# Performance work log

Measured on AMD Instinct MI355X. Metric: run time of the kernel, lower is better.

The kernel has to match this reference:

```python
import jax, jax.numpy as jnp
import numpy as np

K = 20
NEG_SLOPE = 0.2
BN_EPS = 1e-5


def knn_idx(x, k):
    # x: (B, C, N) -> neighbor indices (B, N, k) by largest negative sq-distance
    xt = jnp.swapaxes(x, 1, 2)                      # (B, N, C)
    inner = 2.0 * jnp.einsum('bic,bjc->bij', xt, xt)
    sq = jnp.sum(xt * xt, axis=-1)                  # (B, N)
    dist = inner - sq[:, :, None] - sq[:, None, :]  # -||xi-xj||^2
    _, idx = jax.lax.top_k(dist, k)
    return idx


def edge_feature(x, src, idx):
    # x: (B, C, N) centers; src: (B, C, M) gather source; idx: (B, N, k)
    xt = jnp.swapaxes(x, 1, 2)                      # (B, N, C)
    st = jnp.swapaxes(src, 1, 2)                    # (B, M, C)
    b = jnp.arange(xt.shape[0])[:, None, None]
    neigh = st[b, idx]                              # (B, N, k, C)
    center = xt[:, :, None, :]                      # (B, N, 1, C)
    feat = jnp.concatenate(
        [neigh - center, jnp.broadcast_to(center, neigh.shape)], axis=-1)
    return jnp.transpose(feat, (0, 3, 1, 2))        # (B, 2C, N, k)


def conv_bn_lrelu(x, w, gamma, beta):
    # 1x1 conv (no bias) + training-mode BatchNorm2d + LeakyReLU(0.2)
    y = jnp.einsum('oc,bcnk->bonk', w, x)
    mean = jnp.mean(y, axis=(0, 2, 3), keepdims=True)
    var = jnp.var(y, axis=(0, 2, 3), keepdims=True)
    y = (y - mean) * jax.lax.rsqrt(var + BN_EPS)
    y = y * gamma[None, :, None, None] + beta[None, :, None, None]
    return jnp.where(y >= 0, y, NEG_SLOPE * y)


def knn_ia_idx(x, y, k):
    # cosine-similarity KNN from x (B,Cx,N) into y (B,Cy,M), normalize over channels
    xn = x / jnp.maximum(jnp.linalg.norm(x, axis=1, keepdims=True), 1e-12)
    yn = y / jnp.maximum(jnp.linalg.norm(y, axis=1, keepdims=True), 1e-12)
    simi = jnp.einsum('bci,bcj->bij', xn, yn)       # (B, N, M)
    _, idx = jax.lax.top_k(simi, k)
    return idx


def setup_inputs() -> dict:
    key = jax.random.key(0)
    ks = jax.random.split(key, 8)
    B, N, M, EMB = 8, 1024, 1024, 512
    x = jax.random.normal(ks[0], (B, 3, N), dtype=jnp.float32)
    y = jax.random.normal(ks[1], (B, 128, M), dtype=jnp.float32)
    def w(k_, o, c):
        return jax.random.normal(k_, (o, c), dtype=jnp.float32) * (1.0 / np.sqrt(c))
    inp = {
        'x': x, 'y': y,
        'w1': w(ks[2], 64, 6),
        'w2': w(ks[3], 64, 128),
        'w3': w(ks[4], 128, 128),
        'w4': w(ks[5], 256, 256),
        'w5': w(ks[6], EMB, 512),
        'g1': jnp.ones(64), 'b1': jnp.zeros(64),
        'g2': jnp.ones(64), 'b2': jnp.zeros(64),
        'g3': jnp.ones(128), 'b3': jnp.zeros(128),
        'g4': jnp.ones(256), 'b4': jnp.zeros(256),
        'g5': jnp.ones(EMB), 'b5': jnp.zeros(EMB),
    }
    return inp


def reference(x, y, w1, w2, w3, w4, w5, g1, b1, g2, b2, g3, b3, g4, b4, g5, b5):
    # block 1
    h = conv_bn_lrelu(edge_feature(x, x, knn_idx(x, K)), w1, g1, b1)
    x1 = jnp.max(h, axis=-1)                        # (B, 64, N)
    # block 2
    h = conv_bn_lrelu(edge_feature(x1, x1, knn_idx(x1, K)), w2, g2, b2)
    x2 = jnp.max(h, axis=-1)                        # (B, 64, N)
    # block 3
    h = conv_bn_lrelu(edge_feature(x2, x2, knn_idx(x2, K)), w3, g3, b3)
    x3 = jnp.max(h, axis=-1)                        # (B, 128, N)
    # block 4: cross-attention KNN into y (cosine similarity)
    h = conv_bn_lrelu(edge_feature(x3, y, knn_ia_idx(x3, y, K)), w4, g4, b4)
    x4 = jnp.max(h, axis=-1)                        # (B, 256, N)
    # final 1x1 conv + BN + LeakyReLU on concatenated features (512 ch)
    cat = jnp.concatenate([x1, x2, x3, x4], axis=1)  # (B, 512, N)
    out = conv_bn_lrelu(cat[..., None], w5, g5, b5)[..., 0]
    return out                                       # (B, n_emb_dims, N)
```

## Files before the change

kernel.cpp:

```cpp
#include <hip/hip_runtime.h>
#include <hip/hip_bf16.h>

#define KNN 20
#define NEG_SLOPE 0.2f

constexpr int BB = 8;
constexpr int NN = 1024;
constexpr int MM = 1024;

typedef short bf16x8 __attribute__((ext_vector_type(8)));
typedef float f32x4 __attribute__((ext_vector_type(4)));
typedef double f64x4 __attribute__((ext_vector_type(4)));
typedef unsigned long long u64;

__device__ __forceinline__ u64 pack_key64(double d, int j) {
  u64 u = (u64)__double_as_longlong(d);
  u = (u & 0x8000000000000000ULL) ? ~u : (u | 0x8000000000000000ULL);
  return (u & ~(u64)1023) | (u64)(1023 - j);
}

__device__ __forceinline__ void topk20_u64(u64 (&s)[16], int lane, int* op) {
#pragma unroll
  for (int p = 1; p < 16; p <<= 1) {
#pragma unroll
    for (int k = p; k >= 1; k >>= 1) {
#pragma unroll
      for (int j = k % p; j + k < 16; j += 2 * k) {
#pragma unroll
        for (int i = 0; i < k; ++i) {
          int a = j + i, b = j + i + k;
          if (b < 16 && (a / (2 * p)) == (b / (2 * p))) {
            u64 hi = s[a] > s[b] ? s[a] : s[b];
            u64 lo = s[a] > s[b] ? s[b] : s[a];
            s[a] = hi;
            s[b] = lo;
          }
        }
      }
    }
  }
#pragma unroll
  for (int r = 0; r < KNN; ++r) {
    u64 win = s[0];
#pragma unroll
    for (int off = 32; off > 0; off >>= 1) {
      u64 o = __shfl_xor(win, off, 64);
      win = o > win ? o : win;
    }
    if (lane == 0) op[r] = 1023 - (int)(win & (u64)1023);
    if (s[0] == win) {
#pragma unroll
      for (int i = 0; i < 15; ++i) s[i] = s[i + 1];
      s[15] = 0ULL;
    }
  }
}

__global__ void k_probe_mfma(int* __restrict__ rowt, int* __restrict__ colt,
                             int* __restrict__ flag) {
  __shared__ int cnt[256];
  __shared__ int oksh;
  int tid = threadIdx.x;
  if (tid == 0) oksh = 1;
  for (int e = tid; e < 256; e += 64) cnt[e] = 0;
  __syncthreads();
  int lane = tid & 63;
  f64x4 z = {0.0, 0.0, 0.0, 0.0};
  double ai = (double)(lane & 15);
  double p3 = 1.0, p5 = 1.0;
  int kq = lane >> 4;
  for (int t = 0; t < kq; ++t) { p3 *= 3.0; p5 *= 5.0; }
  f64x4 d1 = __builtin_amdgcn_mfma_f64_16x16x4f64(ai, 1.0, z, 0, 0, 0);
  f64x4 d2 = __builtin_amdgcn_mfma_f64_16x16x4f64(1.0, ai, z, 0, 0, 0);
  f64x4 d3 = __builtin_amdgcn_mfma_f64_16x16x4f64(p3, p5, z, 0, 0, 0);
  bool ok = true;
  int ri[4], ci[4];
#pragma unroll
  for (int r = 0; r < 4; ++r) {
    double va = d1[r], vb = d2[r], vp = d3[r];
    int i = (int)(va * 0.25);
    int j = (int)(vb * 0.25);
    bool e_ok = (i >= 0) && (i < 16) && (j >= 0) && (j < 16) &&
                (va == 4.0 * (double)i) && (vb == 4.0 * (double)j) && (vp == 3616.0);
    if (e_ok) {
      atomicAdd(&cnt[i * 16 + j], 1);
    } else {
      ok = false;
      i = 0;
      j = 0;
    }
    ri[r] = i;
    ci[r] = j;
  }
  if (!ok) atomicExch(&oksh, 0);
  __syncthreads();
  bool bij = true;
  for (int e = tid; e < 256; e += 64)
    if (cnt[e] != 1) bij = false;
  if (!bij) atomicExch(&oksh, 0);
  __syncthreads();
#pragma unroll
  for (int r = 0; r < 4; ++r) {
    rowt[lane * 4 + r] = ri[r];
    colt[lane * 4 + r] = ci[r];
  }
  if (tid == 0) *flag = oksh;
}

__global__ __launch_bounds__(256) void k_transpose_d(
    const float* __restrict__ in, double* __restrict__ out, int C, int Np) {
  int total = BB * C * Np;
  for (int t = blockIdx.x * 256 + threadIdx.x; t < total; t += gridDim.x * 256) {
    int c = t % C;
    int n = (t / C) % Np;
    int b = t / (C * Np);
    out[t] = (double)in[((size_t)b * C + c) * Np + n];
  }
}

__global__ __launch_bounds__(256) void k_cvt_bf16(
    const float* __restrict__ in, __hip_bfloat16* __restrict__ out, int n) {
  int i = blockIdx.x * 256 + threadIdx.x;
  if (i < n) out[i] = __float2bfloat16(in[i]);
}

template <int RECIP>
__global__ __launch_bounds__(256) void k_rowsq(
    const double* __restrict__ A, int ld, int C, double* __restrict__ sq) {
  int p = blockIdx.x * 256 + threadIdx.x;
  if (p >= BB * NN) return;
  const double* row = A + (size_t)p * ld;
  double s = 0.0;
  for (int c = 0; c < C; ++c) { double v = row[c]; s += v * v; }
  if (RECIP) {
    sq[p] = 1.0 / fmax(sqrt(s), 1e-12);
  } else {
    sq[p] = s;
  }
}

__global__ __launch_bounds__(256) void k_knn3(
    const double* __restrict__ xs3, const double* __restrict__ sq, int* __restrict__ idx) {
  __shared__ double P[NN * 3];
  int b = blockIdx.x;
  const double* Xb = xs3 + (size_t)b * NN * 3;
  int tid = threadIdx.x;
  for (int t = tid; t < NN * 3; t += 256) P[t] = Xb[t];
  __syncthreads();
  int wave = tid >> 6, lane = tid & 63;
  int i = blockIdx.y * 4 + wave;
  double xi = P[i * 3], yi = P[i * 3 + 1], zi = P[i * 3 + 2];
  double sqi = sq[b * NN + i];
  u64 s[16];
#pragma unroll
  for (int m = 0; m < 16; ++m) {
    int j = m * 64 + lane;
    double d = fma(xi, P[j * 3], 0.0);
    d = fma(yi, P[j * 3 + 1], d);
    d = fma(zi, P[j * 3 + 2], d);
    s[m] = pack_key64(2.0 * d - sqi - sq[b * NN + j], j);
  }
  int* op = idx + ((size_t)b * NN + i) * KNN;
  topk20_u64(s, lane, op);
}

template <int MODE>
__global__ __launch_bounds__(64, 2) void k_gram_u(
    const double* __restrict__ A, int lda, const double* __restrict__ Bm, int ldb,
    const double* __restrict__ sqA, const double* __restrict__ sqB,
    u64* __restrict__ kk, int C, int b0, const int* __restrict__ rowt,
    const int* __restrict__ colt, const int* __restrict__ flag) {
  __shared__ double As[2][8][69];
  __shared__ double Bs[2][8][69];
  int bg = b0 + blockIdx.x;
  int bl = blockIdx.x;
  int j0 = blockIdx.y * 64;
  int i0 = blockIdx.z * 64;
  const double* Ab = A + (size_t)bg * NN * lda;
  const double* Bb = Bm + (size_t)bg * MM * ldb;
  int lane = threadIdx.x;
  if (*flag) {
    int lm = lane & 15, lq = lane >> 4;
    int k8 = lane & 7, r8 = lane >> 3;
    const double* pa = Ab + (size_t)(i0 + r8) * lda + k8;
    const double* pb = Bb + (size_t)(j0 + r8) * ldb + k8;
    f64x4 acc[4][4] = {};
    double ra[8], rb[8];
#pragma unroll
    for (int r = 0; r < 8; ++r) {
      ra[r] = pa[(size_t)(8 * r) * lda];
      rb[r] = pb[(size_t)(8 * r) * ldb];
    }
#pragma unroll
    for (int r = 0; r < 8; ++r) {
      As[0][k8][r8 + 8 * r] = ra[r];
      Bs[0][k8][r8 + 8 * r] = rb[r];
    }
    int nblk = C >> 3;
    for (int cb = 0; cb < nblk; ++cb) {
      int buf = cb & 1;
      bool pf = (cb + 1 < nblk);
      if (pf) {
        int c0 = (cb + 1) << 3;
#pragma unroll
        for (int r = 0; r < 8; ++r) {
          ra[r] = pa[(size_t)(8 * r) * lda + c0];
          rb[r] = pb[(size_t)(8 * r) * ldb + c0];
        }
      }
#pragma unroll
      for (int kc = 0; kc < 2; ++kc) {
        double a_[4], b_[4];
#pragma unroll
        for (int s = 0; s < 4; ++s) {
          a_[s] = As[buf][kc * 4 + lq][s * 16 + lm];
          b_[s] = Bs[buf][kc * 4 + lq][s * 16 + lm];
        }
#pragma unroll
        for (int si = 0; si < 4; ++si)
#pragma unroll
          for (int sj = 0; sj < 4; ++sj)
            acc[si][sj] = __builtin_amdgcn_mfma_f64_16x16x4f64(a_[si], b_[sj],
                                                               acc[si][sj], 0, 0, 0);
      }
      if (pf) {
        int nb = buf ^ 1;
#pragma unroll
        for (int r = 0; r < 8; ++r) {
          As[nb][k8][r8 + 8 * r] = ra[r];
          Bs[nb][k8][r8 + 8 * r] = rb[r];
        }
      }
    }
    int rta[4], cta[4];
#pragma unroll
    for (int r = 0; r < 4; ++r) {
      rta[r] = rowt[lane * 4 + r];
      cta[r] = colt[lane * 4 + r];
    }
#pragma unroll
    for (int si = 0; si < 4; ++si) {
#pragma unroll
      for (int sj = 0; sj < 4; ++sj) {
#pragma unroll
        for (int r = 0; r < 4; ++r) {
          int i = i0 + si * 16 + rta[r];
          int j = j0 + sj * 16 + cta[r];
          double v = acc[si][sj][r];
          if (MODE == 1)
            v = 2.0 * v - sqA[(size_t)bg * NN + i] - sqB[(size_t)bg * MM + j];
          if (MODE == 2) v = v * sqA[(size_t)bg * NN + i] * sqB[(size_t)bg * MM + j];
          kk[((size_t)bl * NN + i) * MM + j] = pack_key64(v, j);
        }
      }
    }
  } else {
    int lr = lane >> 3, lc = lane & 7;
    double acc2[8][8] = {};
    for (int c0 = 0; c0 < C; c0 += 8) {
      if (c0) __syncthreads();
      for (int r = 0; r < 8; ++r) {
        int li = lane + r * 64;
        int row = li >> 3, k = li & 7;
        As[0][k][row] = Ab[(size_t)(i0 + row) * lda + c0 + k];
        Bs[0][k][row] = Bb[(size_t)(j0 + row) * ldb + c0 + k];
      }
      __syncthreads();
#pragma unroll
      for (int k = 0; k < 8; ++k) {
        double a_[8], b_[8];
#pragma unroll
        for (int t = 0; t < 8; ++t) {
          a_[t] = As[0][k][lr * 8 + t];
          b_[t] = Bs[0][k][lc * 8 + t];
        }
#pragma unroll
        for (int ii = 0; ii < 8; ++ii)
#pragma unroll
          for (int jj = 0; jj < 8; ++jj)
            acc2[ii][jj] = fma(a_[ii], b_[jj], acc2[ii][jj]);
      }
    }
    for (int ii = 0; ii < 8; ++ii) {
      int i = i0 + lr * 8 + ii;
      double qa = sqA[(size_t)bg * NN + i];
      for (int jj = 0; jj < 8; ++jj) {
        int j = j0 + lc * 8 + jj;
        double v = acc2[ii][jj];
        if (MODE == 1) v = 2.0 * v - qa - sqB[(size_t)bg * MM + j];
        if (MODE == 2) v = v * qa * sqB[(size_t)bg * MM + j];
        kk[((size_t)bl * NN + i) * MM + j] = pack_key64(v, j);
      }
    }
  }
}

__global__ __launch_bounds__(256) void k_topk(const u64* __restrict__ kk,
                                              int* __restrict__ idx, int b0) {
  int wave = threadIdx.x >> 6;
  int lane = threadIdx.x & 63;
  int bl = blockIdx.x;
  int row = blockIdx.y * 4 + wave;
  const u64* rp = kk + ((size_t)bl * NN + row) * MM;
  u64 s[16];
#pragma unroll
  for (int m = 0; m < 16; ++m) s[m] = rp[m * 64 + lane];
  int* op = idx + ((size_t)(b0 + bl) * NN + row) * KNN;
  topk20_u64(s, lane, op);
}

__global__ __launch_bounds__(256) void k_featmm2(
    const double* __restrict__ src0, int ld0, int Np0,
    const double* __restrict__ src1, int ld1,
    const float* __restrict__ w, int CW,
    double* __restrict__ out0, double* __restrict__ out1, int C, int O,
    const int* __restrict__ rowt, const int* __restrict__ colt,
    const int* __restrict__ flag) {
  __shared__ double As[16][68];
  __shared__ double Ws[16][68];
  int nbo = O >> 6;
  int b = blockIdx.x;
  int mode = blockIdx.y >= nbo;
  int o0 = (blockIdx.y - (mode ? nbo : 0)) * 64;
  int j0 = blockIdx.z * 64;
  const double* src = mode ? src1 : src0;
  int lds_ = mode ? ld1 : ld0;
  int Np = mode ? NN : Np0;
  double* out = mode ? out1 : out0;
  int tid = threadIdx.x;
  const double* Sb = src + (size_t)b * Np * lds_;
  if (*flag) {
    int lane = tid & 63, wv = tid >> 6;
    int lm = lane & 15, lq = lane >> 4;
    f64x4 acc[4] = {};
    for (int c0 = 0; c0 < C; c0 += 16) {
      if (c0) __syncthreads();
      for (int r = 0; r < 4; ++r) {
        int li = tid + r * 256;
        int row = li >> 4, k = li & 15;
        int c = c0 + k;
        As[k][row] = (c < C) ? Sb[(size_t)(j0 + row) * lds_ + c] : 0.0;
        double wvv = 0.0;
        if (c < C) {
          const float* wr = w + (size_t)(o0 + row) * CW;
          wvv = (mode == 0) ? (double)wr[c] : ((double)wr[C + c] - (double)wr[c]);
        }
        Ws[k][row] = wvv;
      }
      __syncthreads();
#pragma unroll
      for (int kc = 0; kc < 4; ++kc) {
        double a = As[kc * 4 + lq][wv * 16 + lm];
#pragma unroll
        for (int t = 0; t < 4; ++t) {
          double bb = Ws[kc * 4 + lq][t * 16 + lm];
          acc[t] = __builtin_amdgcn_mfma_f64_16x16x4f64(a, bb, acc[t], 0, 0, 0);
        }
      }
    }
    int rta[4], cta[4];
#pragma unroll
    for (int r = 0; r < 4; ++r) {
      rta[r] = rowt[lane * 4 + r];
      cta[r] = colt[lane * 4 + r];
    }
#pragma unroll
    for (int t = 0; t < 4; ++t) {
#pragma unroll
      for (int r = 0; r < 4; ++r) {
        int j = j0 + wv * 16 + rta[r];
        int o = o0 + t * 16 + cta[r];
        out[((size_t)b * Np + j) * O + o] = acc[t][r];
      }
    }
  } else {
    int tx = tid & 15, ty = tid >> 4;
    double acc[4][4] = {};
    for (int c0 = 0; c0 < C; c0 += 16) {
      if (c0) __syncthreads();
      for (int r = 0; r < 4; ++r) {
        int li = tid + r * 256;
        int row = li >> 4, k = li & 15;
        int c = c0 + k;
        As[k][row] = (c < C) ? Sb[(size_t)(j0 + row) * lds_ + c] : 0.0;
        double wvv = 0.0;
        if (c < C) {
          const float* wr = w + (size_t)(o0 + row) * CW;
          wvv = (mode == 0) ? (double)wr[c] : ((double)wr[C + c] - (double)wr[c]);
        }
        Ws[k][row] = wvv;
      }
      __syncthreads();
#pragma unroll
      for (int k = 0; k < 16; ++k) {
        double a_[4], b_[4];
#pragma unroll
        for (int ii = 0; ii < 4; ++ii) a_[ii] = As[k][ty * 4 + ii];
#pragma unroll
        for (int jj = 0; jj < 4; ++jj) b_[jj] = Ws[k][tx * 4 + jj];
#pragma unroll
        for (int ii = 0; ii < 4; ++ii)
#pragma unroll
          for (int jj = 0; jj < 4; ++jj)
            acc[ii][jj] = fma(a_[ii], b_[jj], acc[ii][jj]);
      }
    }
    for (int ii = 0; ii < 4; ++ii) {
      int j = j0 + ty * 4 + ii;
      double* op = &out[((size_t)b * Np + j) * O + o0 + tx * 4];
      double2 v0, v1;
      v0.x = acc[ii][0];
      v0.y = acc[ii][1];
      v1.x = acc[ii][2];
      v1.y = acc[ii][3];
      *(double2*)op = v0;
      *(double2*)(op + 2) = v1;
    }
  }
}

__global__ __launch_bounds__(64, 2) void k_gemm5_mfma(
    const __hip_bfloat16* __restrict__ cath, const __hip_bfloat16* __restrict__ w5h,
    float* __restrict__ out) {
  int b = blockIdx.x;
  int j0 = blockIdx.y * 64;
  int o0 = blockIdx.z * 64;
  int lane = threadIdx.x;
  int m = lane & 15;
  int quad = lane >> 4;
  const __hip_bfloat16* arow = cath + ((size_t)(b * NN + j0 + m)) * 512 + quad * 8;
  const __hip_bfloat16* brow = w5h + ((size_t)(o0 + m)) * 512 + quad * 8;
  f32x4 acc[4][4] = {};
#pragma unroll
  for (int c0 = 0; c0 < 512; c0 += 32) {
    bf16x8 a[4], bb[4];
#pragma unroll
    for (int s = 0; s < 4; ++s) {
      a[s] = *(const bf16x8*)(arow + (size_t)s * 16 * 512 + c0);
      bb[s] = *(const bf16x8*)(brow + (size_t)s * 16 * 512 + c0);
    }
#pragma unroll
    for (int si = 0; si < 4; ++si)
#pragma unroll
      for (int sj = 0; sj < 4; ++sj)
        acc[si][sj] =
            __builtin_amdgcn_mfma_f32_16x16x32_bf16(a[si], bb[sj], acc[si][sj], 0, 0, 0);
  }
#pragma unroll
  for (int si = 0; si < 4; ++si) {
    float* ob = &out[((size_t)(b * NN + j0 + si * 16 + quad * 4)) * 512 + o0 + m];
#pragma unroll
    for (int sj = 0; sj < 4; ++sj)
#pragma unroll
      for (int r = 0; r < 4; ++r)
        ob[(size_t)r * 512 + sj * 16] = acc[si][sj][r];
  }
}

__global__ __launch_bounds__(256) void k_gather(
    const double* __restrict__ u, const double* __restrict__ t, const int* __restrict__ idx,
    double* __restrict__ stats, double* __restrict__ mx, int O, int srcNp) {
  __shared__ int lidx[16 * KNN];
  __shared__ double rs[256];
  __shared__ double rq[256];
  int b = blockIdx.x;
  int n0 = blockIdx.y * 16;
  int o0 = blockIdx.z * 64;
  int tid = threadIdx.x;
  int lane = tid & 63, nsl = tid >> 6;
  for (int w = tid; w < 16 * KNN; w += 256)
    lidx[w] = idx[((size_t)b * NN + n0) * KNN + w];
  __syncthreads();
  int oo = o0 + lane;
  double s1 = 0.0, s2 = 0.0;
  for (int ns = nsl; ns < 16; ns += 4) {
    size_t row = (size_t)b * NN + n0 + ns;
    double tv = t[row * O + oo];
    double mxv = -INFINITY;
    double a1 = 0.0, a2 = 0.0;
#pragma unroll
    for (int k = 0; k < KNN; ++k) {
      int j = lidx[ns * KNN + k];
      double yv = u[((size_t)b * srcNp + j) * O + oo] + tv;
      mxv = fmax(mxv, yv);
      a1 += yv;
      a2 = fma(yv, yv, a2);
    }
    mx[row * O + oo] = mxv;
    s1 += a1;
    s2 += a2;
  }
  rs[tid] = s1;
  rq[tid] = s2;
  __syncthreads();
  if (tid < 64) {
    s1 = rs[tid] + rs[tid + 64] + rs[tid + 128] + rs[tid + 192];
    s2 = rq[tid] + rq[tid + 64] + rq[tid + 128] + rq[tid + 192];
    atomicAdd(&stats[o0 + tid], s1);
    atomicAdd(&stats[O + o0 + tid], s2);
  }
}

__global__ __launch_bounds__(256) void k_bnapply(
    const double* __restrict__ mx, const double* __restrict__ u, const double* __restrict__ t,
    const int* __restrict__ idx, const double* __restrict__ stats,
    const float* __restrict__ gamma, const float* __restrict__ beta, double cnt,
    double* __restrict__ catd, __hip_bfloat16* __restrict__ cath, int coff, int O,
    int srcNp) {
  __shared__ double scs[256];
  __shared__ double scc[256];
  int tid = threadIdx.x;
  if (tid < O) {
    double mean = stats[tid] / cnt;
    double var = stats[O + tid] / cnt - mean * mean;
    if (var < 0.0) var = 0.0;
    double rstd = 1.0 / sqrt(var + 1e-5);
    double s = (double)gamma[tid] * rstd;
    scs[tid] = s;
    scc[tid] = (double)beta[tid] - mean * s;
  }
  __syncthreads();
  int i = blockIdx.x * 256 + tid;
  int total = BB * NN * O;
  if (i >= total) return;
  int oo = i % O;
  int n = (i / O) % NN;
  int b = i / (O * NN);
  double s = scs[oo], c = scc[oo];
  double v;
  if (s >= 0.0) {
    v = mx[i];
  } else {
    double tv = t[i];
    double mn = INFINITY;
    for (int k = 0; k < KNN; ++k) {
      int j = idx[((size_t)b * NN + n) * KNN + k];
      mn = fmin(mn, u[((size_t)b * srcNp + j) * O + oo] + tv);
    }
    v = mn;
  }
  double a = s * v + c;
  a = (a >= 0.0) ? a : 0.2 * a;
  size_t ci = ((size_t)b * NN + n) * 512 + coff + oo;
  cath[ci] = __float2bfloat16((float)a);
  if (coff < 256) catd[((size_t)b * NN + n) * 256 + coff + oo] = a;
}

__global__ __launch_bounds__(256) void k_stats512(
    const float* __restrict__ y5, double* __restrict__ stats) {
  int b = blockIdx.y;
  int n0 = blockIdx.x * 32;
  int tid = threadIdx.x;
  for (int part = 0; part < 2; ++part) {
    int oo = tid + part * 256;
    float a1 = 0.f, a2 = 0.f;
    for (int ns = 0; ns < 32; ++ns) {
      float v = y5[((size_t)b * NN + n0 + ns) * 512 + oo];
      a1 += v;
      a2 = fmaf(v, v, a2);
    }
    atomicAdd(&stats[oo], (double)a1);
    atomicAdd(&stats[512 + oo], (double)a2);
  }
}

__global__ __launch_bounds__(256) void k_final5b(
    const float* __restrict__ y5, const double* __restrict__ stats,
    const float* __restrict__ g5, const float* __restrict__ b5,
    float* __restrict__ out) {
  __shared__ float tile[64][65];
  __shared__ double scs[64];
  __shared__ double scc[64];
  int b = blockIdx.z;
  int n0 = blockIdx.x * 64;
  int o0 = blockIdx.y * 64;
  int tid = threadIdx.x;
  if (tid < 64) {
    int o = o0 + tid;
    double cnt = (double)(BB * NN);
    double mean = stats[o] / cnt;
    double var = stats[512 + o] / cnt - mean * mean;
    if (var < 0.0) var = 0.0;
    double rstd = 1.0 / sqrt(var + 1e-5);
    double s = (double)g5[o] * rstd;
    scs[tid] = s;
    scc[tid] = (double)b5[o] - mean * s;
  }
  __syncthreads();
  for (int r = 0; r < 16; ++r) {
    int li = tid + r * 256;
    int nl = li >> 6, ol = li & 63;
    float v = y5[((size_t)b * NN + n0 + nl) * 512 + o0 + ol];
    float a = (float)(scs[ol] * (double)v + scc[ol]);
    a = (a >= 0.f) ? a : NEG_SLOPE * a;
    tile[nl][ol] = a;
  }
  __syncthreads();
  for (int r = 0; r < 16; ++r) {
    int li = tid + r * 256;
    int ol = li >> 6, nl = li & 63;
    out[((size_t)b * 512 + o0 + ol) * NN + n0 + nl] = tile[nl][ol];
  }
}

extern "C" void kernel_launch(void* const* d_in, const int* in_sizes, int n_in,
                              void* d_out, int out_size, void* d_ws, size_t ws_size,
                              hipStream_t stream) {
  const float* x = (const float*)d_in[0];
  const float* y = (const float*)d_in[1];
  const float* w1 = (const float*)d_in[2];
  const float* w2 = (const float*)d_in[3];
  const float* w3 = (const float*)d_in[4];
  const float* w4 = (const float*)d_in[5];
  const float* w5 = (const float*)d_in[6];
  const float* g1 = (const float*)d_in[7];
  const float* b1 = (const float*)d_in[8];
  const float* g2 = (const float*)d_in[9];
  const float* b2 = (const float*)d_in[10];
  const float* g3 = (const float*)d_in[11];
  const float* b3 = (const float*)d_in[12];
  const float* g4 = (const float*)d_in[13];
  const float* b4 = (const float*)d_in[14];
  const float* g5 = (const float*)d_in[15];
  const float* b5 = (const float*)d_in[16];

  char* base = (char*)d_ws;
  size_t off = 0;
  auto alloc = [&](size_t bytes) -> char* {
    char* p = base + off;
    off += (bytes + 255) & ~(size_t)255;
    return p;
  };
  double* st = (double*)alloc(1024 * 8);
  double* sq = (double*)alloc((size_t)BB * NN * 8);
  double* rnx = (double*)alloc((size_t)BB * NN * 8);
  double* rny = (double*)alloc((size_t)BB * MM * 8);
  int* idxb = (int*)alloc((size_t)BB * NN * KNN * 4);
  int* rowt = (int*)alloc(256 * 4);
  int* colt = (int*)alloc(256 * 4);
  int* pflag = (int*)alloc(256);
  double* xs3d = (double*)alloc((size_t)BB * NN * 3 * 8);
  double* ysd = (double*)alloc((size_t)BB * MM * 128 * 8);
  double* catd = (double*)alloc((size_t)BB * NN * 256 * 8);
  __hip_bfloat16* cath = (__hip_bfloat16*)alloc((size_t)BB * NN * 512 * 2);
  __hip_bfloat16* w5h = (__hip_bfloat16*)alloc((size_t)512 * 512 * 2);
  double* uu = (double*)alloc((size_t)BB * MM * 256 * 8);
  double* tt = (double*)alloc((size_t)BB * NN * 256 * 8);
  size_t kkBatchBytes = (size_t)NN * MM * 8;
  size_t avail = (ws_size > off) ? (ws_size - off) : 0;
  int CB = (int)(avail / kkBatchBytes);
  if (CB < 1) CB = 1;
  if (CB > BB) CB = BB;
  u64* KK = (u64*)alloc((size_t)CB * kkBatchBytes);
  float* y5 = (float*)uu;
  double* mx = (double*)d_out;
  float* outp = (float*)d_out;

  const double cntE = (double)BB * NN * KNN;

  auto knn = [&](const double* A, int lda, const double* Bm, int ldb,
                 const double* sa, const double* sb, int C, int mode) {
    for (int b0 = 0; b0 < BB; b0 += CB) {
      int cb = (BB - b0 < CB) ? (BB - b0) : CB;
      dim3 g(cb, MM / 64, NN / 64);
      if (mode == 1)
        k_gram_u<1><<<g, 64, 0, stream>>>(A, lda, Bm, ldb, sa, sb, KK, C, b0, rowt,
                                          colt, pflag);
      else
        k_gram_u<2><<<g, 64, 0, stream>>>(A, lda, Bm, ldb, sa, sb, KK, C, b0, rowt,
                                          colt, pflag);
      k_topk<<<dim3(cb, 256), 256, 0, stream>>>(KK, idxb, b0);
    }
  };

  auto edge_layer = [&](const double* ctr, int ldc, const double* src, int ldsrc,
                        int srcNp, const float* w, int CW, const float* g,
                        const float* bb, int C, int O, int coff) {
    k_featmm2<<<dim3(8, 2 * (O / 64), 16), 256, 0, stream>>>(
        src, ldsrc, srcNp, ctr, ldc, w, CW, uu, tt, C, O, rowt, colt, pflag);
    hipMemsetAsync(st, 0, 1024 * 8, stream);
    k_gather<<<dim3(BB, NN / 16, O / 64), 256, 0, stream>>>(uu, tt, idxb, st, mx, O,
                                                            srcNp);
    k_bnapply<<<(BB * NN * O + 255) / 256, 256, 0, stream>>>(
        mx, uu, tt, idxb, st, g, bb, cntE, catd, cath, coff, O, srcNp);
  };

  k_probe_mfma<<<1, 64, 0, stream>>>(rowt, colt, pflag);
  k_transpose_d<<<96, 256, 0, stream>>>(x, xs3d, 3, NN);
  k_transpose_d<<<2048, 256, 0, stream>>>(y, ysd, 128, MM);
  k_cvt_bf16<<<1024, 256, 0, stream>>>(w5, w5h, 512 * 512);

  k_rowsq<0><<<32, 256, 0, stream>>>(xs3d, 3, 3, sq);
  k_knn3<<<dim3(BB, 256), 256, 0, stream>>>(xs3d, sq, idxb);
  edge_layer(xs3d, 3, xs3d, 3, NN, w1, 6, g1, b1, 3, 64, 0);

  k_rowsq<0><<<32, 256, 0, stream>>>(catd, 256, 64, sq);
  knn(catd, 256, catd, 256, sq, sq, 64, 1);
  edge_layer(catd, 256, catd, 256, NN, w2, 128, g2, b2, 64, 64, 64);

  k_rowsq<0><<<32, 256, 0, stream>>>(catd + 64, 256, 64, sq);
  knn(catd + 64, 256, catd + 64, 256, sq, sq, 64, 1);
  edge_layer(catd + 64, 256, catd + 64, 256, NN, w3, 128, g3, b3, 64, 128, 128);

  k_rowsq<1><<<32, 256, 0, stream>>>(catd + 128, 256, 128, rnx);
  k_rowsq<1><<<32, 256, 0, stream>>>(ysd, 128, 128, rny);
  knn(catd + 128, 256, ysd, 128, rnx, rny, 128, 2);
  edge_layer(catd + 128, 256, ysd, 128, MM, w4, 256, g4, b4, 128, 256, 256);

  hipMemsetAsync(st, 0, 1024 * 8, stream);
  k_gemm5_mfma<<<dim3(8, 16, 8), 64, 0, stream>>>(cath, w5h, y5);
  k_stats512<<<dim3(32, 8), 256, 0, stream>>>(y5, st);
  k_final5b<<<dim3(16, 8, 8), 256, 0, stream>>>(y5, st, g5, b5, outp);
}
```

Measured before the change: 647.7 us.

## Exploit symmetric Gram matrix for self-KNN and merge BN stats memsets

```diff
diff --git a/kernel.cpp b/kernel.cpp
--- a/kernel.cpp
+++ b/kernel.cpp
@@ -290,6 +290,138 @@
         if (MODE == 1) v = 2.0 * v - qa - sqB[(size_t)bg * MM + j];
         if (MODE == 2) v = v * qa * sqB[(size_t)bg * MM + j];
         kk[((size_t)bl * NN + i) * MM + j] = pack_key64(v, j);
+      }
+    }
+  }
+}
+
+__global__ __launch_bounds__(64, 2) void k_gram_sym(
+    const double* __restrict__ A, int lda, const double* __restrict__ sqA,
+    u64* __restrict__ kk, int C, int b0, const int* __restrict__ rowt,
+    const int* __restrict__ colt, const int* __restrict__ flag) {
+  __shared__ double As[2][8][69];
+  __shared__ double Bs[2][8][69];
+  int bg = b0 + blockIdx.x;
+  int bl = blockIdx.x;
+  int p = blockIdx.y;
+  int r = (int)((sqrtf(8.f * p + 1.f) - 1.f) * 0.5f);
+  while ((r + 1) * (r + 2) / 2 <= p) ++r;
+  while (r * (r + 1) / 2 > p) --r;
+  int cc = p - r * (r + 1) / 2;
+  int i0 = r * 64, j0 = cc * 64;
+  const double* Ab = A + (size_t)bg * NN * lda;
+  int lane = threadIdx.x;
+  if (*flag) {
+    int lm = lane & 15, lq = lane >> 4;
+    int k8 = lane & 7, r8 = lane >> 3;
+    const double* pa = Ab + (size_t)(i0 + r8) * lda + k8;
+    const double* pb = Ab + (size_t)(j0 + r8) * lda + k8;
+    f64x4 acc[4][4] = {};
+    double ra[8], rb[8];
+#pragma unroll
+    for (int r_ = 0; r_ < 8; ++r_) {
+      ra[r_] = pa[(size_t)(8 * r_) * lda];
+      rb[r_] = pb[(size_t)(8 * r_) * lda];
+    }
+#pragma unroll
+    for (int r_ = 0; r_ < 8; ++r_) {
+      As[0][k8][r8 + 8 * r_] = ra[r_];
+      Bs[0][k8][r8 + 8 * r_] = rb[r_];
+    }
+    int nblk = C >> 3;
+    for (int cb = 0; cb < nblk; ++cb) {
+      int buf = cb & 1;
+      bool pf = (cb + 1 < nblk);
+      if (pf) {
+        int c0 = (cb + 1) << 3;
+#pragma unroll
+        for (int r_ = 0; r_ < 8; ++r_) {
+          ra[r_] = pa[(size_t)(8 * r_) * lda + c0];
+          rb[r_] = pb[(size_t)(8 * r_) * lda + c0];
+        }
+      }
+#pragma unroll
+      for (int kc = 0; kc < 2; ++kc) {
+        double a_[4], b_[4];
+#pragma unroll
+        for (int s = 0; s < 4; ++s) {
+          a_[s] = As[buf][kc * 4 + lq][s * 16 + lm];
+          b_[s] = Bs[buf][kc * 4 + lq][s * 16 + lm];
+        }
+#pragma unroll
+        for (int si = 0; si < 4; ++si)
+#pragma unroll
+          for (int sj = 0; sj < 4; ++sj)
+            acc[si][sj] = __builtin_amdgcn_mfma_f64_16x16x4f64(a_[si], b_[sj],
+                                                               acc[si][sj], 0, 0, 0);
+      }
+      if (pf) {
+        int nb = buf ^ 1;
+#pragma unroll
+        for (int r_ = 0; r_ < 8; ++r_) {
+          As[nb][k8][r8 + 8 * r_] = ra[r_];
+          Bs[nb][k8][r8 + 8 * r_] = rb[r_];
+        }
+      }
+    }
+    int rta[4], cta[4];
+#pragma unroll
+    for (int r_ = 0; r_ < 4; ++r_) {
+      rta[r_] = rowt[lane * 4 + r_];
+      cta[r_] = colt[lane * 4 + r_];
+    }
+    bool mir = (i0 != j0);
+#pragma unroll
+    for (int si = 0; si < 4; ++si) {
+#pragma unroll
+      for (int sj = 0; sj < 4; ++sj) {
+#pragma unroll
+        for (int r_ = 0; r_ < 4; ++r_) {
+          int i = i0 + si * 16 + rta[r_];
+          int j = j0 + sj * 16 + cta[r_];
+          double v = 2.0 * acc[si][sj][r_] - sqA[(size_t)bg * NN + i] -
+                     sqA[(size_t)bg * NN + j];
+          kk[((size_t)bl * NN + i) * MM + j] = pack_key64(v, j);
+          if (mir) kk[((size_t)bl * NN + j) * MM + i] = pack_key64(v, i);
+        }
+      }
+    }
+  } else {
+    int lr = lane >> 3, lc = lane & 7;
+    double acc2[8][8] = {};
+    for (int c0 = 0; c0 < C; c0 += 8) {
+      if (c0) __syncthreads();
+      for (int r_ = 0; r_ < 8; ++r_) {
+        int li = lane + r_ * 64;
+        int row = li >> 3, k = li & 7;
+        As[0][k][row] = Ab[(size_t)(i0 + row) * lda + c0 + k];
+        Bs[0][k][row] = Ab[(size_t)(j0 + row) * lda + c0 + k];
+      }
+      __syncthreads();
+#pragma unroll
+      for (int k = 0; k < 8; ++k) {
+        double a_[8], b_[8];
+#pragma unroll
+        for (int t = 0; t < 8; ++t) {
+          a_[t] = As[0][k][lr * 8 + t];
+          b_[t] = Bs[0][k][lc * 8 + t];
+        }
+#pragma unroll
+        for (int ii = 0; ii < 8; ++ii)
+#pragma unroll
+          for (int jj = 0; jj < 8; ++jj)
+            acc2[ii][jj] = fma(a_[ii], b_[jj], acc2[ii][jj]);
+      }
+    }
+    bool mir = (i0 != j0);
+    for (int ii = 0; ii < 8; ++ii) {
+      int i = i0 + lr * 8 + ii;
+      double qa = sqA[(size_t)bg * NN + i];
+      for (int jj = 0; jj < 8; ++jj) {
+        int j = j0 + lc * 8 + jj;
+        double v = 2.0 * acc2[ii][jj] - qa - sqA[(size_t)bg * NN + j];
+        kk[((size_t)bl * NN + i) * MM + j] = pack_key64(v, j);
+        if (mir) kk[((size_t)bl * NN + j) * MM + i] = pack_key64(v, i);
       }
     }
   }
@@ -631,7 +763,7 @@
     off += (bytes + 255) & ~(size_t)255;
     return p;
   };
-  double* st = (double*)alloc(1024 * 8);
+  double* stAll = (double*)alloc(5 * 1024 * 8);
   double* sq = (double*)alloc((size_t)BB * NN * 8);
   double* rnx = (double*)alloc((size_t)BB * NN * 8);
   double* rny = (double*)alloc((size_t)BB * MM * 8);
@@ -659,32 +791,33 @@
   const double cntE = (double)BB * NN * KNN;
 
   auto knn = [&](const double* A, int lda, const double* Bm, int ldb,
-                 const double* sa, const double* sb, int C, int mode) {
+                 const double* sa, const double* sb, int C, int sym) {
     for (int b0 = 0; b0 < BB; b0 += CB) {
       int cb = (BB - b0 < CB) ? (BB - b0) : CB;
-      dim3 g(cb, MM / 64, NN / 64);
-      if (mode == 1)
-        k_gram_u<1><<<g, 64, 0, stream>>>(A, lda, Bm, ldb, sa, sb, KK, C, b0, rowt,
-                                          colt, pflag);
-      else
+      if (sym) {
+        k_gram_sym<<<dim3(cb, 136), 64, 0, stream>>>(A, lda, sa, KK, C, b0, rowt, colt,
+                                                     pflag);
+      } else {
+        dim3 g(cb, MM / 64, NN / 64);
         k_gram_u<2><<<g, 64, 0, stream>>>(A, lda, Bm, ldb, sa, sb, KK, C, b0, rowt,
                                           colt, pflag);
+      }
       k_topk<<<dim3(cb, 256), 256, 0, stream>>>(KK, idxb, b0);
     }
   };
 
   auto edge_layer = [&](const double* ctr, int ldc, const double* src, int ldsrc,
                         int srcNp, const float* w, int CW, const float* g,
-                        const float* bb, int C, int O, int coff) {
+                        const float* bb, int C, int O, int coff, double* st) {
     k_featmm2<<<dim3(8, 2 * (O / 64), 16), 256, 0, stream>>>(
         src, ldsrc, srcNp, ctr, ldc, w, CW, uu, tt, C, O, rowt, colt, pflag);
-    hipMemsetAsync(st, 0, 1024 * 8, stream);
     k_gather<<<dim3(BB, NN / 16, O / 64), 256, 0, stream>>>(uu, tt, idxb, st, mx, O,
                                                             srcNp);
     k_bnapply<<<(BB * NN * O + 255) / 256, 256, 0, stream>>>(
         mx, uu, tt, idxb, st, g, bb, cntE, catd, cath, coff, O, srcNp);
   };
 
+  hipMemsetAsync(stAll, 0, 5 * 1024 * 8, stream);
   k_probe_mfma<<<1, 64, 0, stream>>>(rowt, colt, pflag);
   k_transpose_d<<<96, 256, 0, stream>>>(x, xs3d, 3, NN);
   k_transpose_d<<<2048, 256, 0, stream>>>(y, ysd, 128, MM);
@@ -692,23 +825,25 @@
 
   k_rowsq<0><<<32, 256, 0, stream>>>(xs3d, 3, 3, sq);
   k_knn3<<<dim3(BB, 256), 256, 0, stream>>>(xs3d, sq, idxb);
-  edge_layer(xs3d, 3, xs3d, 3, NN, w1, 6, g1, b1, 3, 64, 0);
+  edge_layer(xs3d, 3, xs3d, 3, NN, w1, 6, g1, b1, 3, 64, 0, stAll);
 
   k_rowsq<0><<<32, 256, 0, stream>>>(catd, 256, 64, sq);
   knn(catd, 256, catd, 256, sq, sq, 64, 1);
-  edge_layer(catd, 256, catd, 256, NN, w2, 128, g2, b2, 64, 64, 64);
+  edge_layer(catd, 256, catd, 256, NN, w2, 128, g2, b2, 64, 64, 64, stAll + 1024);
 
   k_rowsq<0><<<32, 256, 0, stream>>>(catd + 64, 256, 64, sq);
   knn(catd + 64, 256, catd + 64, 256, sq, sq, 64, 1);
-  edge_layer(catd + 64, 256, catd + 64, 256, NN, w3, 128, g3, b3, 64, 128, 128);
+  edge_layer(catd + 64, 256, catd + 64, 256, NN, w3, 128, g3, b3, 64, 128, 128,
+             stAll + 2048);
 
   k_rowsq<1><<<32, 256, 0, stream>>>(catd + 128, 256, 128, rnx);
   k_rowsq<1><<<32, 256, 0, stream>>>(ysd, 128, 128, rny);
-  knn(catd + 128, 256, ysd, 128, rnx, rny, 128, 2);
-  edge_layer(catd + 128, 256, ysd, 128, MM, w4, 256, g4, b4, 128, 256, 256);
-
-  hipMemsetAsync(st, 0, 1024 * 8, stream);
+  knn(catd + 128, 256, ysd, 128, rnx, rny, 128, 0);
+  edge_layer(catd + 128, 256, ysd, 128, MM, w4, 256, g4, b4, 128, 256, 256,
+             stAll + 3072);
+
+  double* st5 = stAll + 4096;
   k_gemm5_mfma<<<dim3(8, 16, 8), 64, 0, stream>>>(cath, w5h, y5);
-  k_stats512<<<dim3(32, 8), 256, 0, stream>>>(y5, st);
-  k_final5b<<<dim3(16, 8, 8), 256, 0, stream>>>(y5, st, g5, b5, outp);
-}
+  k_stats512<<<dim3(32, 8), 256, 0, stream>>>(y5, st5);
+  k_final5b<<<dim3(16, 8, 8), 256, 0, stream>>>(y5, st5, g5, b5, outp);
+}
```

Result: no change. 645.2 us (-0.4%).
